# Optimization experiments

Measured on AMD Instinct MI355X. Metric: run time of the kernel, lower is better.

Reference implementation:

```python
import jax, jax.numpy as jnp
import numpy as np

N, F, K, D = 4096, 512, 8, 64


def setup_inputs() -> dict:
    key = jax.random.key(0)
    ks = jax.random.split(key, 6)
    H = jax.random.normal(ks[0], (N, F), dtype=jnp.float32)
    # dense 0/1 adjacency with self-loops
    A = jax.random.randint(ks[1], (N, N), 0, 2).astype(jnp.float32)
    A = jnp.maximum(A, jnp.eye(N, dtype=jnp.float32))
    idx = jnp.arange(N, dtype=jnp.int64)
    glorot_w = (2.0 / (F + D)) ** 0.5
    glorot_a = (2.0 / (D + 1)) ** 0.5
    kernels = glorot_w * jax.random.normal(ks[2], (K, F, D), dtype=jnp.float32)
    attn_kernels = glorot_a * jax.random.normal(ks[3], (K, 2, D, 1), dtype=jnp.float32)
    biases = 0.01 * jax.random.normal(ks[4], (K, D), dtype=jnp.float32)
    return {"H": H, "A": A, "idx": idx, "kernels": kernels,
            "attn_kernels": attn_kernels, "biases": biases}


def reference(H, A, idx, kernels, attn_kernels, biases):
    # (dropout is identity at inference)
    batch_A = A[:, idx]                                  # [N, N]
    HW = jnp.einsum('nf,kfd->knd', H, kernels)           # [K, N, D]
    a1 = attn_kernels[:, 0, :, 0]                        # [K, D]
    a2 = attn_kernels[:, 1, :, 0]                        # [K, D]
    s1 = jnp.einsum('knd,kd->kn', HW, a1)                # score_i (source)
    s2 = jnp.einsum('knd,kd->kn', HW, a2)                # score_j (target)
    scores = s1[:, :, None] + s2[:, None, :]             # [K, N, N]
    neg_big = jnp.finfo(jnp.float32).min
    scores = jnp.where(batch_A[None, :, :] == 0.0, neg_big, scores)
    # LeakyReLU(0.2) applied AFTER masking, as in the original
    scores = jnp.where(scores >= 0, scores, 0.2 * scores)
    attn = jax.nn.softmax(scores, axis=-1)               # [K, N, N]
    res = jnp.einsum('kij,kjd->kid', attn, HW) + biases[:, None, :]  # [K, N, D]
    out = jax.nn.elu(res)                                # is_last=False -> concat heads
    out = jnp.transpose(out, (1, 0, 2)).reshape(N, K * D)
    return out
```

## Files before the change

kernel.cpp:

```cpp
#include <hip/hip_runtime.h>
#include <hip/hip_fp16.h>
#include <float.h>
#include <math.h>

#define NN 4096
#define FF 512
#define KK 8
#define DD 64

typedef float f32x4 __attribute__((ext_vector_type(4)));
typedef _Float16 f16x4 __attribute__((ext_vector_type(4)));
typedef _Float16 f16x8 __attribute__((ext_vector_type(8)));

__global__ __launch_bounds__(256) void k_bits(const float* __restrict__ A,
                                              unsigned long long* __restrict__ bits) {
  const int gw   = (blockIdx.x * 256 + threadIdx.x) >> 6;
  const int lane = threadIdx.x & 63;
  const int nw   = (gridDim.x * 256) >> 6;
  const int totw = NN * NN / 64;
  for (int wd = gw; wd < totw; wd += nw) {
    float a = A[(size_t)wd * 64 + lane];
    unsigned long long m = __ballot(a != 0.0f);
    if (lane == 0) bits[wd] = m;
  }
}

__global__ __launch_bounds__(256) void k_hf(const float* __restrict__ H,
                                            _Float16* __restrict__ HF) {
  const int w = threadIdx.x >> 6, lane = threadIdx.x & 63;
  const int tile = blockIdx.x * 4 + w;
  const int rb = tile >> 4, fb = tile & 15;
  const int l15 = lane & 15, grp = lane >> 4;
  const float* src = H + (size_t)(rb * 16 + l15) * FF + fb * 32 + grp * 4;
  float4 lo = *reinterpret_cast<const float4*>(src);
  float4 hi = *reinterpret_cast<const float4*>(src + 16);
  f16x8 v;
  v[0] = (_Float16)lo.x; v[1] = (_Float16)lo.y; v[2] = (_Float16)lo.z; v[3] = (_Float16)lo.w;
  v[4] = (_Float16)hi.x; v[5] = (_Float16)hi.y; v[6] = (_Float16)hi.z; v[7] = (_Float16)hi.w;
  *reinterpret_cast<f16x8*>(HF + (size_t)tile * 512 + lane * 8) = v;
}

__global__ __launch_bounds__(256) void k_wf(const float* __restrict__ Wk,
                                            _Float16* __restrict__ WF) {
  const int g = blockIdx.x * 256 + threadIdx.x;
  const int frag = g >> 6, lane = g & 63;
  const int k = frag >> 6, fb = (frag >> 2) & 15, db = frag & 3;
  const int l15 = lane & 15, grp = lane >> 4;
  f16x8 v;
  #pragma unroll
  for (int e = 0; e < 8; ++e) {
    int f = fb * 32 + grp * 4 + (e & 3) + 16 * (e >> 2);
    int d = db * 16 + l15;
    v[e] = (_Float16)Wk[((size_t)k * FF + f) * DD + d];
  }
  *reinterpret_cast<f16x8*>(WF + (size_t)frag * 512 + lane * 8) = v;
}

__global__ __launch_bounds__(256) void k_hw(const _Float16* __restrict__ HF,
                                            const _Float16* __restrict__ WF,
                                            const float* __restrict__ attk,
                                            _Float16* __restrict__ HWF,
                                            float* __restrict__ s1,
                                            float* __restrict__ s2,
                                            float* __restrict__ e2p,
                                            float* __restrict__ e2n) {
  const int w = threadIdx.x >> 6, lane = threadIdx.x & 63;
  const int k = blockIdx.y;
  const int rb = blockIdx.x * 4 + w;
  const int l15 = lane & 15, grp = lane >> 4;
  f32x4 acc[4] = {};
  for (int fb = 0; fb < 16; ++fb) {
    f16x8 a = *reinterpret_cast<const f16x8*>(HF + (size_t)(rb * 16 + fb) * 512 + lane * 8);
    #pragma unroll
    for (int n = 0; n < 4; ++n) {
      f16x8 b = *reinterpret_cast<const f16x8*>(WF + (size_t)((k * 16 + fb) * 4 + n) * 512 + lane * 8);
      acc[n] = __builtin_amdgcn_mfma_f32_16x16x32_f16(a, b, acc[n], 0, 0, 0);
    }
  }
  const int jb = rb >> 1;
  const int half = rb & 1;
  #pragma unroll
  for (int db = 0; db < 4; ++db) {
    f16x4 v;
    #pragma unroll
    for (int q = 0; q < 4; ++q) v[q] = (_Float16)acc[db][q];
    *reinterpret_cast<f16x4*>(HWF + (size_t)((k * 128 + jb) * 4 + db) * 512 + lane * 8 + half * 4) = v;
  }
  float a1v[4], a2v[4];
  #pragma unroll
  for (int n = 0; n < 4; ++n) {
    a1v[n] = attk[k * 2 * DD + n * 16 + l15];
    a2v[n] = attk[k * 2 * DD + DD + n * 16 + l15];
  }
  #pragma unroll
  for (int q = 0; q < 4; ++q) {
    float p1 = 0.f, p2 = 0.f;
    #pragma unroll
    for (int n = 0; n < 4; ++n) { p1 += acc[n][q] * a1v[n]; p2 += acc[n][q] * a2v[n]; }
    #pragma unroll
    for (int off = 8; off; off >>= 1) { p1 += __shfl_xor(p1, off); p2 += __shfl_xor(p2, off); }
    if (l15 == 0) {
      int row = rb * 16 + grp * 4 + q;
      s1[k * NN + row]  = p1;
      s2[k * NN + row]  = p2;
      e2p[k * NN + row] = __expf(p2);
      e2n[k * NN + row] = __expf(0.2f * p2);
    }
  }
}

__global__ __launch_bounds__(256) void k_mx(const float* __restrict__ s2,
                                            float* __restrict__ mx) {
  const int k = blockIdx.x, tid = threadIdx.x;
  float m = -FLT_MAX;
  for (int j = tid; j < NN; j += 256) m = fmaxf(m, s2[k * NN + j]);
  #pragma unroll
  for (int o = 32; o; o >>= 1) m = fmaxf(m, __shfl_xor(m, o));
  __shared__ float sm[4];
  if ((tid & 63) == 0) sm[tid >> 6] = m;
  __syncthreads();
  if (tid == 0) mx[k] = fmaxf(fmaxf(sm[0], sm[1]), fmaxf(sm[2], sm[3]));
}

__global__ __launch_bounds__(256, 4) void k_attn(
    const unsigned long long* __restrict__ bits,
    const _Float16* __restrict__ HWF,
    const float* __restrict__ s1, const float* __restrict__ s2,
    const float* __restrict__ e2p, const float* __restrict__ e2n,
    const float* __restrict__ mx,
    float* __restrict__ pacc, float* __restrict__ pw) {
  __shared__ __align__(16) float s2l[2048], epl[2048], enl[2048];
  const int k = blockIdx.y, jh = blockIdx.z;
  const int i0 = blockIdx.x * 64;
  const int tid = threadIdx.x;
  const int w = tid >> 6, lane = tid & 63, l15 = lane & 15, grp = lane >> 4;
  const int jbase = jh * 2048;
  for (int t = tid; t < 512; t += 256) {
    *reinterpret_cast<float4*>(&s2l[t * 4]) = *reinterpret_cast<const float4*>(&s2[k * NN + jbase + t * 4]);
    *reinterpret_cast<float4*>(&epl[t * 4]) = *reinterpret_cast<const float4*>(&e2p[k * NN + jbase + t * 4]);
    *reinterpret_cast<float4*>(&enl[t * 4]) = *reinterpret_cast<const float4*>(&e2n[k * NN + jbase + t * 4]);
  }
  __syncthreads();
  const int row = i0 + w * 16 + l15;
  const float s1r = s1[k * NN + row];
  float cr = s1r + mx[k]; cr = fmaxf(cr, 0.2f * cr);
  const float P1 = __expf(s1r - cr), Q1 = __expf(0.2f * s1r - cr);
  const unsigned long long* brow = bits + (size_t)row * (NN / 64) + (jbase >> 6);
  f32x4 acc[4] = {};
  float wsum = 0.f;
  unsigned long long bw = brow[0];
  for (int jw = 0; jw < 32; ++jw) {
    unsigned long long bwn = brow[jw < 31 ? jw + 1 : 31];
    #pragma unroll
    for (int js = 0; js < 2; ++js) {
      unsigned int m32 = (unsigned int)(bw >> (js * 32));
      const int jl = jw * 64 + js * 32;
      float4 sl = *reinterpret_cast<const float4*>(&s2l[jl + grp * 4]);
      float4 sh = *reinterpret_cast<const float4*>(&s2l[jl + 16 + grp * 4]);
      float4 pl = *reinterpret_cast<const float4*>(&epl[jl + grp * 4]);
      float4 ph = *reinterpret_cast<const float4*>(&epl[jl + 16 + grp * 4]);
      float4 ql = *reinterpret_cast<const float4*>(&enl[jl + grp * 4]);
      float4 qh = *reinterpret_cast<const float4*>(&enl[jl + 16 + grp * 4]);
      unsigned int mg  = m32 >> (grp * 4);
      unsigned int mgh = m32 >> (16 + grp * 4);
      f16x8 af;
      #pragma unroll
      for (int e = 0; e < 4; ++e) {
        float s  = s1r + ((const float*)&sl)[e];
        float v  = s >= 0.f ? P1 * ((const float*)&pl)[e] : Q1 * ((const float*)&ql)[e];
        v = ((mg >> e) & 1u) ? v : 0.f;
        wsum += v; af[e] = (_Float16)v;
        float s2_ = s1r + ((const float*)&sh)[e];
        float v2  = s2_ >= 0.f ? P1 * ((const float*)&ph)[e] : Q1 * ((const float*)&qh)[e];
        v2 = ((mgh >> e) & 1u) ? v2 : 0.f;
        wsum += v2; af[4 + e] = (_Float16)v2;
      }
      const int jbg = jh * 64 + jw * 2 + js;
      #pragma unroll
      for (int n = 0; n < 4; ++n) {
        f16x8 bf = *reinterpret_cast<const f16x8*>(HWF + (size_t)((k * 128 + jbg) * 4 + n) * 512 + lane * 8);
        acc[n] = __builtin_amdgcn_mfma_f32_16x16x32_f16(af, bf, acc[n], 0, 0, 0);
      }
    }
    bw = bwn;
  }
  wsum += __shfl_xor(wsum, 16);
  wsum += __shfl_xor(wsum, 32);
  const size_t pbase = (size_t)jh * KK * NN * DD;
  #pragma unroll
  for (int n = 0; n < 4; ++n)
    #pragma unroll
    for (int q = 0; q < 4; ++q)
      pacc[pbase + ((size_t)k * NN + i0 + w * 16 + grp * 4 + q) * DD + n * 16 + l15] = acc[n][q];
  if (grp == 0) pw[(size_t)jh * KK * NN + k * NN + row] = wsum;
}

__global__ __launch_bounds__(256) void k_merge(const float* __restrict__ pacc,
                                               const float* __restrict__ pw,
                                               const float* __restrict__ bias,
                                               float* __restrict__ out) {
  const int o4 = blockIdx.x * 256 + threadIdx.x;
  const int i = o4 >> 7, rem = o4 & 127, k = rem >> 4, d4 = rem & 15;
  const size_t half = (size_t)KK * NN * DD;
  const size_t idx = ((size_t)k * NN + i) * DD + d4 * 4;
  float4 a0 = *reinterpret_cast<const float4*>(pacc + idx);
  float4 a1 = *reinterpret_cast<const float4*>(pacc + half + idx);
  float rw = 1.0f / (pw[k * NN + i] + pw[KK * NN + k * NN + i]);
  float4 bv = *reinterpret_cast<const float4*>(bias + k * DD + d4 * 4);
  float4 r;
  r.x = (a0.x + a1.x) * rw + bv.x; r.x = r.x > 0.f ? r.x : expm1f(r.x);
  r.y = (a0.y + a1.y) * rw + bv.y; r.y = r.y > 0.f ? r.y : expm1f(r.y);
  r.z = (a0.z + a1.z) * rw + bv.z; r.z = r.z > 0.f ? r.z : expm1f(r.z);
  r.w = (a0.w + a1.w) * rw + bv.w; r.w = r.w > 0.f ? r.w : expm1f(r.w);
  *reinterpret_cast<float4*>(out + (size_t)o4 * 4) = r;
}

extern "C" void kernel_launch(void* const* d_in, const int* in_sizes, int n_in,
                              void* d_out, int out_size, void* d_ws, size_t ws_size,
                              hipStream_t stream) {
  const float* H    = (const float*)d_in[0];
  const float* A    = (const float*)d_in[1];
  const float* Wk   = (const float*)d_in[3];
  const float* attk = (const float*)d_in[4];
  const float* bias = (const float*)d_in[5];
  float* out = (float*)d_out;

  char* base = (char*)d_ws;
  _Float16* HF  = (_Float16*)(base + 0);
  _Float16* WF  = (_Float16*)(base + 4194304);
  _Float16* HWF = (_Float16*)(base + 4718592);
  unsigned long long* bits = (unsigned long long*)(base + 8912896);
  float* s1p  = (float*)(base + 11010048);
  float* s2p  = (float*)(base + 11141120);
  float* e2pp = (float*)(base + 11272192);
  float* e2np = (float*)(base + 11403264);
  float* mxp  = (float*)(base + 11534336);
  float* pacc = (float*)(base + 11534592);
  float* pwp  = (float*)(base + 28311808);

  k_bits<<<2048, 256, 0, stream>>>(A, bits);
  k_hf<<<1024, 256, 0, stream>>>(H, HF);
  k_wf<<<128, 256, 0, stream>>>(Wk, WF);
  k_hw<<<dim3(NN / 64, KK), 256, 0, stream>>>(HF, WF, attk, HWF, s1p, s2p, e2pp, e2np);
  k_mx<<<KK, 256, 0, stream>>>(s2p, mxp);
  k_attn<<<dim3(NN / 64, KK, 2), 256, 0, stream>>>(bits, HWF, s1p, s2p, e2pp, e2np, mxp, pacc, pwp);
  k_merge<<<2048, 256, 0, stream>>>(pacc, pwp, bias, out);
}
```

Measured before the change: 197.7 us.

## Retile attention kernel with packed fp16 softmax weights and 4-way j split

Each attention wave now handles 64 rows (four 16-row subtiles), so every HWF B-fragment load feeds four MFMAs instead of one. The j dimension is split four ways and the per-block LDS tables shrink to fp16 exp values computed in-kernel. Weights are built with packed half2 max/multiply and bitmask ANDs, and row sums use fdot2. Partial accumulators are stored as fp16 to halve merge traffic, and W fragments are staged in LDS in k_hw. The risks are lower occupancy (launch bounds 2), extra fp16 rounding in weights and partials, and only 128 blocks per j-slice.

```diff
diff --git a/kernel.cpp b/kernel.cpp
--- a/kernel.cpp
+++ b/kernel.cpp
@@ -9,18 +9,28 @@
 #define DD 64
 
 typedef float f32x4 __attribute__((ext_vector_type(4)));
+typedef _Float16 h2 __attribute__((ext_vector_type(2)));
 typedef _Float16 f16x4 __attribute__((ext_vector_type(4)));
 typedef _Float16 f16x8 __attribute__((ext_vector_type(8)));
+typedef unsigned int u32;
+typedef unsigned long long u64;
+
+__device__ __forceinline__ h2 H2(u32 u) { union { u32 u; h2 h; } x; x.u = u; return x.h; }
+__device__ __forceinline__ u32 U32(h2 h) { union { u32 u; h2 h; } x; x.h = h; return x.u; }
+__device__ __forceinline__ u32 pmask(u32 m, int sh) {
+  u32 b = (m >> sh) & 3u;
+  return ((b * 0x10001u) & 0x20001u) * 0xFFFFu;
+}
 
 __global__ __launch_bounds__(256) void k_bits(const float* __restrict__ A,
-                                              unsigned long long* __restrict__ bits) {
-  const int gw   = (blockIdx.x * 256 + threadIdx.x) >> 6;
+                                              u64* __restrict__ bits) {
+  const int gw = (blockIdx.x * 256 + threadIdx.x) >> 6;
   const int lane = threadIdx.x & 63;
-  const int nw   = (gridDim.x * 256) >> 6;
+  const int nw = (gridDim.x * 256) >> 6;
   const int totw = NN * NN / 64;
   for (int wd = gw; wd < totw; wd += nw) {
     float a = A[(size_t)wd * 64 + lane];
-    unsigned long long m = __ballot(a != 0.0f);
+    u64 m = __ballot(a != 0.0f);
     if (lane == 0) bits[wd] = m;
   }
 }
@@ -61,19 +71,26 @@
                                             const float* __restrict__ attk,
                                             _Float16* __restrict__ HWF,
                                             float* __restrict__ s1,
-                                            float* __restrict__ s2,
-                                            float* __restrict__ e2p,
-                                            float* __restrict__ e2n) {
+                                            float* __restrict__ s2) {
+  __shared__ __align__(16) _Float16 Bs[64 * 512];
   const int w = threadIdx.x >> 6, lane = threadIdx.x & 63;
   const int k = blockIdx.y;
   const int rb = blockIdx.x * 4 + w;
   const int l15 = lane & 15, grp = lane >> 4;
+  const _Float16* wfk = WF + (size_t)k * 64 * 512;
+  #pragma unroll
+  for (int c = 0; c < 16; ++c) {
+    int chunk = c * 4 + w;
+    *reinterpret_cast<f16x8*>(&Bs[chunk * 512 + lane * 8]) =
+        *reinterpret_cast<const f16x8*>(wfk + (size_t)chunk * 512 + lane * 8);
+  }
+  __syncthreads();
   f32x4 acc[4] = {};
   for (int fb = 0; fb < 16; ++fb) {
     f16x8 a = *reinterpret_cast<const f16x8*>(HF + (size_t)(rb * 16 + fb) * 512 + lane * 8);
     #pragma unroll
     for (int n = 0; n < 4; ++n) {
-      f16x8 b = *reinterpret_cast<const f16x8*>(WF + (size_t)((k * 16 + fb) * 4 + n) * 512 + lane * 8);
+      f16x8 b = *reinterpret_cast<const f16x8*>(&Bs[(fb * 4 + n) * 512 + lane * 8]);
       acc[n] = __builtin_amdgcn_mfma_f32_16x16x32_f16(a, b, acc[n], 0, 0, 0);
     }
   }
@@ -101,10 +118,8 @@
     for (int off = 8; off; off >>= 1) { p1 += __shfl_xor(p1, off); p2 += __shfl_xor(p2, off); }
     if (l15 == 0) {
       int row = rb * 16 + grp * 4 + q;
-      s1[k * NN + row]  = p1;
-      s2[k * NN + row]  = p2;
-      e2p[k * NN + row] = __expf(p2);
-      e2n[k * NN + row] = __expf(0.2f * p2);
+      s1[k * NN + row] = p1;
+      s2[k * NN + row] = p2;
     }
   }
 }
@@ -122,96 +137,135 @@
   if (tid == 0) mx[k] = fmaxf(fmaxf(sm[0], sm[1]), fmaxf(sm[2], sm[3]));
 }
 
-__global__ __launch_bounds__(256, 4) void k_attn(
-    const unsigned long long* __restrict__ bits,
-    const _Float16* __restrict__ HWF,
+__global__ __launch_bounds__(256, 2) void k_attn(
+    const u64* __restrict__ bits, const _Float16* __restrict__ HWF,
     const float* __restrict__ s1, const float* __restrict__ s2,
-    const float* __restrict__ e2p, const float* __restrict__ e2n,
     const float* __restrict__ mx,
-    float* __restrict__ pacc, float* __restrict__ pw) {
-  __shared__ __align__(16) float s2l[2048], epl[2048], enl[2048];
+    _Float16* __restrict__ pacc, float* __restrict__ pw) {
+  __shared__ __align__(16) _Float16 epl[1024];
+  __shared__ __align__(16) _Float16 enl[1024];
   const int k = blockIdx.y, jh = blockIdx.z;
-  const int i0 = blockIdx.x * 64;
+  const int i0 = blockIdx.x * 256;
   const int tid = threadIdx.x;
   const int w = tid >> 6, lane = tid & 63, l15 = lane & 15, grp = lane >> 4;
-  const int jbase = jh * 2048;
-  for (int t = tid; t < 512; t += 256) {
-    *reinterpret_cast<float4*>(&s2l[t * 4]) = *reinterpret_cast<const float4*>(&s2[k * NN + jbase + t * 4]);
-    *reinterpret_cast<float4*>(&epl[t * 4]) = *reinterpret_cast<const float4*>(&e2p[k * NN + jbase + t * 4]);
-    *reinterpret_cast<float4*>(&enl[t * 4]) = *reinterpret_cast<const float4*>(&e2n[k * NN + jbase + t * 4]);
+  const int jbase = jh * 1024;
+  const float mxk = mx[k];
+  {
+    float4 sv = *reinterpret_cast<const float4*>(&s2[k * NN + jbase + tid * 4]);
+    f16x4 e4, n4;
+    e4[0] = (_Float16)__expf(sv.x - mxk); e4[1] = (_Float16)__expf(sv.y - mxk);
+    e4[2] = (_Float16)__expf(sv.z - mxk); e4[3] = (_Float16)__expf(sv.w - mxk);
+    n4[0] = (_Float16)__expf(0.2f * (sv.x - mxk)); n4[1] = (_Float16)__expf(0.2f * (sv.y - mxk));
+    n4[2] = (_Float16)__expf(0.2f * (sv.z - mxk)); n4[3] = (_Float16)__expf(0.2f * (sv.w - mxk));
+    *reinterpret_cast<f16x4*>(&epl[tid * 4]) = e4;
+    *reinterpret_cast<f16x4*>(&enl[tid * 4]) = n4;
   }
   __syncthreads();
-  const int row = i0 + w * 16 + l15;
-  const float s1r = s1[k * NN + row];
-  float cr = s1r + mx[k]; cr = fmaxf(cr, 0.2f * cr);
-  const float P1 = __expf(s1r - cr), Q1 = __expf(0.2f * s1r - cr);
-  const unsigned long long* brow = bits + (size_t)row * (NN / 64) + (jbase >> 6);
-  f32x4 acc[4] = {};
-  float wsum = 0.f;
-  unsigned long long bw = brow[0];
-  for (int jw = 0; jw < 32; ++jw) {
-    unsigned long long bwn = brow[jw < 31 ? jw + 1 : 31];
+  h2 P1h[4], Q1h[4];
+  const u64* browp[4];
+  #pragma unroll
+  for (int s = 0; s < 4; ++s) {
+    int row = i0 + w * 64 + s * 16 + l15;
+    float s1r = s1[k * NN + row];
+    float t = s1r + mxk;
+    float cr = fmaxf(t, 0.2f * t);
+    _Float16 p = (_Float16)__expf(t - cr);
+    _Float16 q = (_Float16)__expf(0.2f * t - cr);
+    P1h[s] = h2{p, p}; Q1h[s] = h2{q, q};
+    browp[s] = bits + (size_t)row * (NN / 64) + (jbase >> 6);
+  }
+  const int g4 = grp * 4;
+  const _Float16* hwb = HWF + ((size_t)(k * 128 + jh * 32) * 4) * 512 + lane * 8;
+  const h2 ones = h2{(_Float16)1.0f, (_Float16)1.0f};
+  f32x4 acc[4][4] = {};
+  float wsum[4] = {};
+  u64 bw[4];
+  #pragma unroll
+  for (int s = 0; s < 4; ++s) bw[s] = browp[s][0];
+  for (int jw = 0; jw < 16; ++jw) {
+    u64 nbw[4];
+    const int nx = jw < 15 ? jw + 1 : 15;
+    #pragma unroll
+    for (int s = 0; s < 4; ++s) nbw[s] = browp[s][nx];
     #pragma unroll
     for (int js = 0; js < 2; ++js) {
-      unsigned int m32 = (unsigned int)(bw >> (js * 32));
       const int jl = jw * 64 + js * 32;
-      float4 sl = *reinterpret_cast<const float4*>(&s2l[jl + grp * 4]);
-      float4 sh = *reinterpret_cast<const float4*>(&s2l[jl + 16 + grp * 4]);
-      float4 pl = *reinterpret_cast<const float4*>(&epl[jl + grp * 4]);
-      float4 ph = *reinterpret_cast<const float4*>(&epl[jl + 16 + grp * 4]);
-      float4 ql = *reinterpret_cast<const float4*>(&enl[jl + grp * 4]);
-      float4 qh = *reinterpret_cast<const float4*>(&enl[jl + 16 + grp * 4]);
-      unsigned int mg  = m32 >> (grp * 4);
-      unsigned int mgh = m32 >> (16 + grp * 4);
-      f16x8 af;
+      f16x8 bf0 = *reinterpret_cast<const f16x8*>(hwb + ((jw * 2 + js) * 4 + 0) * 512);
+      f16x8 bf1 = *reinterpret_cast<const f16x8*>(hwb + ((jw * 2 + js) * 4 + 1) * 512);
+      f16x8 bf2 = *reinterpret_cast<const f16x8*>(hwb + ((jw * 2 + js) * 4 + 2) * 512);
+      f16x8 bf3 = *reinterpret_cast<const f16x8*>(hwb + ((jw * 2 + js) * 4 + 3) * 512);
+      f16x4 elo = *reinterpret_cast<const f16x4*>(&epl[jl + g4]);
+      f16x4 ehi = *reinterpret_cast<const f16x4*>(&epl[jl + 16 + g4]);
+      f16x4 nlo = *reinterpret_cast<const f16x4*>(&enl[jl + g4]);
+      f16x4 nhi = *reinterpret_cast<const f16x4*>(&enl[jl + 16 + g4]);
+      const u32 e01 = ((const u32*)&elo)[0], e23 = ((const u32*)&elo)[1];
+      const u32 e45 = ((const u32*)&ehi)[0], e67 = ((const u32*)&ehi)[1];
+      const u32 n01 = ((const u32*)&nlo)[0], n23 = ((const u32*)&nlo)[1];
+      const u32 n45 = ((const u32*)&nhi)[0], n67 = ((const u32*)&nhi)[1];
       #pragma unroll
-      for (int e = 0; e < 4; ++e) {
-        float s  = s1r + ((const float*)&sl)[e];
-        float v  = s >= 0.f ? P1 * ((const float*)&pl)[e] : Q1 * ((const float*)&ql)[e];
-        v = ((mg >> e) & 1u) ? v : 0.f;
-        wsum += v; af[e] = (_Float16)v;
-        float s2_ = s1r + ((const float*)&sh)[e];
-        float v2  = s2_ >= 0.f ? P1 * ((const float*)&ph)[e] : Q1 * ((const float*)&qh)[e];
-        v2 = ((mgh >> e) & 1u) ? v2 : 0.f;
-        wsum += v2; af[4 + e] = (_Float16)v2;
-      }
-      const int jbg = jh * 64 + jw * 2 + js;
-      #pragma unroll
-      for (int n = 0; n < 4; ++n) {
-        f16x8 bf = *reinterpret_cast<const f16x8*>(HWF + (size_t)((k * 128 + jbg) * 4 + n) * 512 + lane * 8);
-        acc[n] = __builtin_amdgcn_mfma_f32_16x16x32_f16(af, bf, acc[n], 0, 0, 0);
+      for (int s = 0; s < 4; ++s) {
+        const u32 m32 = (u32)(bw[s] >> (js * 32));
+        u32 p0 = U32(__builtin_elementwise_max(P1h[s] * H2(e01), Q1h[s] * H2(n01))) & pmask(m32, g4);
+        u32 p1 = U32(__builtin_elementwise_max(P1h[s] * H2(e23), Q1h[s] * H2(n23))) & pmask(m32, g4 + 2);
+        u32 p2 = U32(__builtin_elementwise_max(P1h[s] * H2(e45), Q1h[s] * H2(n45))) & pmask(m32, g4 + 16);
+        u32 p3 = U32(__builtin_elementwise_max(P1h[s] * H2(e67), Q1h[s] * H2(n67))) & pmask(m32, g4 + 18);
+        wsum[s] = __builtin_amdgcn_fdot2(H2(p0), ones, wsum[s], false);
+        wsum[s] = __builtin_amdgcn_fdot2(H2(p1), ones, wsum[s], false);
+        wsum[s] = __builtin_amdgcn_fdot2(H2(p2), ones, wsum[s], false);
+        wsum[s] = __builtin_amdgcn_fdot2(H2(p3), ones, wsum[s], false);
+        union { u32 u[4]; f16x8 v; } af;
+        af.u[0] = p0; af.u[1] = p1; af.u[2] = p2; af.u[3] = p3;
+        acc[s][0] = __builtin_amdgcn_mfma_f32_16x16x32_f16(af.v, bf0, acc[s][0], 0, 0, 0);
+        acc[s][1] = __builtin_amdgcn_mfma_f32_16x16x32_f16(af.v, bf1, acc[s][1], 0, 0, 0);
+        acc[s][2] = __builtin_amdgcn_mfma_f32_16x16x32_f16(af.v, bf2, acc[s][2], 0, 0, 0);
+        acc[s][3] = __builtin_amdgcn_mfma_f32_16x16x32_f16(af.v, bf3, acc[s][3], 0, 0, 0);
       }
     }
-    bw = bwn;
-  }
-  wsum += __shfl_xor(wsum, 16);
-  wsum += __shfl_xor(wsum, 32);
-  const size_t pbase = (size_t)jh * KK * NN * DD;
-  #pragma unroll
-  for (int n = 0; n < 4; ++n)
-    #pragma unroll
-    for (int q = 0; q < 4; ++q)
-      pacc[pbase + ((size_t)k * NN + i0 + w * 16 + grp * 4 + q) * DD + n * 16 + l15] = acc[n][q];
-  if (grp == 0) pw[(size_t)jh * KK * NN + k * NN + row] = wsum;
-}
-
-__global__ __launch_bounds__(256) void k_merge(const float* __restrict__ pacc,
+    #pragma unroll
+    for (int s = 0; s < 4; ++s) bw[s] = nbw[s];
+  }
+  const size_t ob = (size_t)(jh * KK + k) * NN;
+  #pragma unroll
+  for (int s = 0; s < 4; ++s) {
+    float ws = wsum[s];
+    ws += __shfl_xor(ws, 16);
+    ws += __shfl_xor(ws, 32);
+    #pragma unroll
+    for (int n = 0; n < 4; ++n)
+      #pragma unroll
+      for (int q = 0; q < 4; ++q) {
+        int row = i0 + w * 64 + s * 16 + grp * 4 + q;
+        pacc[(ob + row) * DD + n * 16 + l15] = (_Float16)acc[s][n][q];
+      }
+    if (grp == 0) {
+      int row = i0 + w * 64 + s * 16 + l15;
+      pw[ob + row] = ws;
+    }
+  }
+}
+
+__global__ __launch_bounds__(256) void k_merge(const _Float16* __restrict__ pacc,
                                                const float* __restrict__ pw,
                                                const float* __restrict__ bias,
                                                float* __restrict__ out) {
   const int o4 = blockIdx.x * 256 + threadIdx.x;
   const int i = o4 >> 7, rem = o4 & 127, k = rem >> 4, d4 = rem & 15;
-  const size_t half = (size_t)KK * NN * DD;
   const size_t idx = ((size_t)k * NN + i) * DD + d4 * 4;
-  float4 a0 = *reinterpret_cast<const float4*>(pacc + idx);
-  float4 a1 = *reinterpret_cast<const float4*>(pacc + half + idx);
-  float rw = 1.0f / (pw[k * NN + i] + pw[KK * NN + k * NN + i]);
+  float4 a = {0.f, 0.f, 0.f, 0.f};
+  float wsum = 0.f;
+  #pragma unroll
+  for (int s = 0; s < 4; ++s) {
+    f16x4 v = *reinterpret_cast<const f16x4*>(&pacc[(size_t)s * (KK * NN * DD) + idx]);
+    a.x += (float)v[0]; a.y += (float)v[1]; a.z += (float)v[2]; a.w += (float)v[3];
+    wsum += pw[(size_t)s * (KK * NN) + k * NN + i];
+  }
+  float rw = 1.0f / wsum;
   float4 bv = *reinterpret_cast<const float4*>(bias + k * DD + d4 * 4);
   float4 r;
-  r.x = (a0.x + a1.x) * rw + bv.x; r.x = r.x > 0.f ? r.x : expm1f(r.x);
-  r.y = (a0.y + a1.y) * rw + bv.y; r.y = r.y > 0.f ? r.y : expm1f(r.y);
-  r.z = (a0.z + a1.z) * rw + bv.z; r.z = r.z > 0.f ? r.z : expm1f(r.z);
-  r.w = (a0.w + a1.w) * rw + bv.w; r.w = r.w > 0.f ? r.w : expm1f(r.w);
+  r.x = a.x * rw + bv.x; r.x = r.x > 0.f ? r.x : expm1f(r.x);
+  r.y = a.y * rw + bv.y; r.y = r.y > 0.f ? r.y : expm1f(r.y);
+  r.z = a.z * rw + bv.z; r.z = r.z > 0.f ? r.z : expm1f(r.z);
+  r.w = a.w * rw + bv.w; r.w = r.w > 0.f ? r.w : expm1f(r.w);
   *reinterpret_cast<float4*>(out + (size_t)o4 * 4) = r;
 }
 
@@ -229,20 +283,18 @@
   _Float16* HF  = (_Float16*)(base + 0);
   _Float16* WF  = (_Float16*)(base + 4194304);
   _Float16* HWF = (_Float16*)(base + 4718592);
-  unsigned long long* bits = (unsigned long long*)(base + 8912896);
-  float* s1p  = (float*)(base + 11010048);
-  float* s2p  = (float*)(base + 11141120);
-  float* e2pp = (float*)(base + 11272192);
-  float* e2np = (float*)(base + 11403264);
-  float* mxp  = (float*)(base + 11534336);
-  float* pacc = (float*)(base + 11534592);
-  float* pwp  = (float*)(base + 28311808);
+  u64* bits     = (u64*)(base + 8912896);
+  float* s1p    = (float*)(base + 11010048);
+  float* s2p    = (float*)(base + 11141120);
+  float* mxp    = (float*)(base + 11272192);
+  _Float16* pacc = (_Float16*)(base + 11276288);
+  float* pwp    = (float*)(base + 28053504);
 
   k_bits<<<2048, 256, 0, stream>>>(A, bits);
   k_hf<<<1024, 256, 0, stream>>>(H, HF);
   k_wf<<<128, 256, 0, stream>>>(Wk, WF);
-  k_hw<<<dim3(NN / 64, KK), 256, 0, stream>>>(HF, WF, attk, HWF, s1p, s2p, e2pp, e2np);
+  k_hw<<<dim3(NN / 64, KK), 256, 0, stream>>>(HF, WF, attk, HWF, s1p, s2p);
   k_mx<<<KK, 256, 0, stream>>>(s2p, mxp);
-  k_attn<<<dim3(NN / 64, KK, 2), 256, 0, stream>>>(bits, HWF, s1p, s2p, e2pp, e2np, mxp, pacc, pwp);
+  k_attn<<<dim3(NN / 256, KK, 4), 256, 0, stream>>>(bits, HWF, s1p, s2p, mxp, pacc, pwp);
   k_merge<<<2048, 256, 0, stream>>>(pacc, pwp, bias, out);
 }
```

After: 176.2 us. 10.9% less time.
